# Performance work log

Hardware: AMD Instinct MI355X
Metric: run time of the kernel (lower is better)

The kernel has to match this reference:

```python
import jax, jax.numpy as jnp
import numpy as np

D_MODEL = 512
N_HEADS = 8
D_HEAD = D_MODEL // N_HEADS


def setup_inputs() -> dict:
    key = jax.random.key(0)
    ks = jax.random.split(key, 11)
    B, S = 2, 4096
    scale = 1.0 / np.sqrt(D_MODEL)
    inp = {
        "q": jax.random.normal(ks[0], (B, S, D_MODEL), dtype=jnp.float32),
        "k": jax.random.normal(ks[1], (B, S, D_MODEL), dtype=jnp.float32),
        "v": jax.random.normal(ks[2], (B, S, D_MODEL), dtype=jnp.float32),
        "Wq": jax.random.normal(ks[3], (D_MODEL, D_MODEL), dtype=jnp.float32) * scale,
        "bq": jnp.zeros((D_MODEL,), dtype=jnp.float32),
        "Wk": jax.random.normal(ks[4], (D_MODEL, D_MODEL), dtype=jnp.float32) * scale,
        "bk": jnp.zeros((D_MODEL,), dtype=jnp.float32),
        "Wv": jax.random.normal(ks[5], (D_MODEL, D_MODEL), dtype=jnp.float32) * scale,
        "bv": jnpp if False else jnp.zeros((D_MODEL,), dtype=jnp.float32),
        "Wo": jax.random.normal(ks[6], (D_MODEL, D_MODEL), dtype=jnp.float32) * scale,
        "bo": jnp.zeros((D_MODEL,), dtype=jnp.float32),
    }
    return inp


def reference(q, k, v, Wq, bq, Wk, bk, Wv, bv, Wo, bo):
    B, S, _ = q.shape
    # Linear projections (torch Linear: x @ W^T + b), split into heads -> [B,H,S,Dh]
    def proj(x, W, b):
        y = jnp.einsum("bsd,ed->bse", x, W) + b
        return y.reshape(B, -1, N_HEADS, D_HEAD).transpose(0, 2, 1, 3)

    Q = proj(q, Wq, bq)
    K = proj(k, Wk, bk)
    V = proj(v, Wv, bv)

    inv_sqrt_dh = 1.0 / np.sqrt(D_HEAD).astype(np.float32)
    scores = jnp.einsum("bhqd,bhkd->bhqk", Q, K) * inv_sqrt_dh  # [B,H,S,S]
    attn = jax.nn.softmax(scores, axis=-1)  # dropout is identity at eval
    out = jnp.einsum("bhqk,bhkd->bhqd", attn, V)  # [B,H,S,Dh]
    out = out.transpose(0, 2, 1, 3).reshape(B, S, D_MODEL)
    return jnp.einsum("bsd,ed->bse", out, Wo) + bo
```

## Files before the change

### kernel.cpp

```cpp
#include <hip/hip_runtime.h>
#include <hip/hip_bf16.h>
#include <hip/hip_fp16.h>
#include <stdint.h>

#define D_MODEL 512
#define NH 8
#define DH 64
#define BB 2
#define SS 4096
#define MTOT (BB*SS)
#define NJQ 2

typedef __attribute__((ext_vector_type(8))) short bf16x8;
typedef __attribute__((ext_vector_type(4))) float f32x4;
typedef __fp16 fp16x2 __attribute__((ext_vector_type(2)));

#define MFMA32(a,b,c) __builtin_amdgcn_mfma_f32_16x16x32_bf16(a,b,c,0,0,0)

#if __has_builtin(__builtin_amdgcn_exp2f)
  #define EXP2F(x) __builtin_amdgcn_exp2f(x)
#else
  #define EXP2F(x) __expf((x) * 0.6931471805599453f)
#endif

#define QSCALE 0.18033688011112042f
#define EXPOFF 11.541560327679939f

__device__ __forceinline__ unsigned f2b(float f) {
  return (__float_as_uint(f) + 0x8000u) >> 16;
}
__device__ __forceinline__ float h2f(unsigned short h) {
  return __half2float(__ushort_as_half(h));
}
__device__ __forceinline__ unsigned packh2(float lo, float hi) {
  fp16x2 h = __builtin_amdgcn_cvt_pkrtz(lo, hi);
  return __builtin_bit_cast(unsigned, h);
}
__device__ __forceinline__ unsigned packpair(float lo, float hi) {
  return __builtin_amdgcn_perm(__float_as_uint(hi) + 0x8000u,
                               __float_as_uint(lo) + 0x8000u, 0x07060302u);
}
__device__ __forceinline__ unsigned cvtpk_bf16(float lo, float hi) {
  unsigned r;
  asm("v_cvt_pk_bf16_f32 %0, %1, %2" : "=v"(r) : "v"(lo), "v"(hi));
  return r;
}
__device__ __forceinline__ void gload_lds16(const unsigned short* g, unsigned short* l) {
  __builtin_amdgcn_global_load_lds(
      (const __attribute__((address_space(1))) unsigned int*)g,
      (__attribute__((address_space(3))) unsigned int*)l, 16, 0, 0);
}

struct PrepArgs {
  const float* src[7];
  unsigned short* dst[7];
  int off[8];
};

__global__ __launch_bounds__(256) void prep_kernel(PrepArgs a) {
  const int bx = blockIdx.x;
  int tgt = 0;
#pragma unroll
  for (int s = 1; s < 7; s++) tgt += (bx >= a.off[s]);
  const int i = ((bx - a.off[tgt]) * 256 + threadIdx.x) * 8;
  const float4 f0 = *(const float4*)(a.src[tgt] + i);
  const float4 f1 = *(const float4*)(a.src[tgt] + i + 4);
  uint4 o;
  o.x = packpair(f0.x, f0.y);
  o.y = packpair(f0.z, f0.w);
  o.z = packpair(f1.x, f1.y);
  o.w = packpair(f1.z, f1.w);
  *(uint4*)(a.dst[tgt] + i) = o;
}

struct CombArgs {
  const unsigned short* Os[NJQ];
  const float* ls[NJQ];
  unsigned short* Ao;
};

__global__ __launch_bounds__(256) void combine_kernel(CombArgs c) {
  const size_t i = ((size_t)blockIdx.x * 256 + threadIdx.x) * 8;
  const int m = (int)(i >> 9);
  const int k = (int)(i & 511);
  const int hh = k >> 6;
  float lsum = 0.f;
#pragma unroll
  for (int s = 0; s < NJQ; s++) lsum += c.ls[s][(size_t)m * NH + hh];
  const float inv = __builtin_amdgcn_rcpf(lsum);
  float sum[8] = {0.f, 0.f, 0.f, 0.f, 0.f, 0.f, 0.f, 0.f};
#pragma unroll
  for (int s = 0; s < NJQ; s++) {
    uint4 hv = *(const uint4*)(c.Os[s] + i);
    const unsigned short* he = (const unsigned short*)&hv;
#pragma unroll
    for (int e = 0; e < 8; e++) sum[e] += h2f(he[e]);
  }
  uint4 pk;
  pk.x = packpair(sum[0] * inv, sum[1] * inv);
  pk.y = packpair(sum[2] * inv, sum[3] * inv);
  pk.z = packpair(sum[4] * inv, sum[5] * inv);
  pk.w = packpair(sum[6] * inv, sum[7] * inv);
  *(uint4*)(c.Ao + i) = pk;
}

struct GemmArgs {
  const unsigned short* A[3];
  const unsigned short* W[3];
  const float* bias[3];
  unsigned short* out[3];
  float* outf;
  int mode;
};

__global__ __launch_bounds__(256) void gemm_kernel(GemmArgs g) {
  const int z = blockIdx.z;
  const float* __restrict__ bias = g.bias[z];
  unsigned short* __restrict__ out = g.out[z];
  const bool vt = (g.mode == 0) && (z == 2);
  const float osc = (g.mode == 0 && z == 0) ? QSCALE : 1.0f;

  __shared__ __align__(128) unsigned short lA[128][32];
  __shared__ __align__(128) unsigned short lB[128][32];

  const int t = threadIdx.x;
  const int lane = t & 63;
  const int w = t >> 6;
  const int wr = w >> 1, wc = w & 1;
  const int lrow = lane & 15, quad = lane >> 4;

  const int ob = blockIdx.y * 4 + blockIdx.x;
  const int lid = (ob & 7) * 32 + (ob >> 3);
  const int m0 = (lid >> 2) * 128;
  const int n0 = (lid & 3) * 128;

  const int srow = lane >> 2;
  const int schunk = (lane & 3) * 8;

  const unsigned short* __restrict__ Ag = g.A[z];
  const unsigned short* __restrict__ Wg = g.W[z];

  f32x4 acc[4][4];
  for (int i = 0; i < 4; i++)
    for (int j = 0; j < 4; j++)
      for (int r = 0; r < 4; r++) acc[i][j][r] = 0.f;

  for (int kk = 0; kk < 512; kk += 32) {
#pragma unroll
    for (int i = 0; i < 2; i++) {
      const int r0 = w * 32 + i * 16;
      gload_lds16(Ag + (size_t)(m0 + r0 + srow) * 512 + kk + schunk, &lA[r0][0]);
      gload_lds16(Wg + (size_t)(n0 + r0 + srow) * 512 + kk + schunk, &lB[r0][0]);
    }
    __syncthreads();
    bf16x8 af[4], bfr[4];
#pragma unroll
    for (int mt = 0; mt < 4; mt++) af[mt] = *(const bf16x8*)&lA[wr * 64 + mt * 16 + lrow][quad * 8];
#pragma unroll
    for (int nt = 0; nt < 4; nt++) bfr[nt] = *(const bf16x8*)&lB[wc * 64 + nt * 16 + lrow][quad * 8];
#pragma unroll
    for (int mt = 0; mt < 4; mt++)
#pragma unroll
      for (int nt = 0; nt < 4; nt++)
        acc[mt][nt] = MFMA32(af[mt], bfr[nt], acc[mt][nt]);
    __syncthreads();
  }

  float bv[4];
#pragma unroll
  for (int nt = 0; nt < 4; nt++) bv[nt] = bias[n0 + wc * 64 + nt * 16 + lrow];

#pragma unroll
  for (int mt = 0; mt < 4; mt++) {
#pragma unroll
    for (int nt = 0; nt < 4; nt++) {
      const int n = n0 + wc * 64 + nt * 16 + lrow;
      const int mB = m0 + wr * 64 + mt * 16 + quad * 4;
      float val[4];
#pragma unroll
      for (int r = 0; r < 4; r++) val[r] = (acc[mt][nt][r] + bv[nt]) * osc;

      if (g.mode == 1) {
#pragma unroll
        for (int r = 0; r < 4; r++) g.outf[(size_t)(mB + r) * 512 + n] = val[r];
      } else if (vt) {
        const int bb = mB >> 12, s = mB & 4095;
        const int a = s >> 2;
        const int c0 = (s & ~31) + (a & 4) + ((a & 3) << 3);
        const int hh = n >> 6, dh = n & 63;
        ushort4 pk = make_ushort4((unsigned short)f2b(val[0]), (unsigned short)f2b(val[1]),
                                  (unsigned short)f2b(val[2]), (unsigned short)f2b(val[3]));
        *(ushort4*)(out + (((size_t)bb * NH + hh) * DH + dh) * SS + c0) = pk;
      } else {
        const int bb = mB >> 12;
        const int hh = n >> 6, dh = n & 63;
#pragma unroll
        for (int r = 0; r < 4; r++) {
          const int s = (mB + r) & 4095;
          out[((((size_t)bb * NH + hh) * SS + s) << 6) + dh] = (unsigned short)f2b(val[r]);
        }
      }
    }
  }
}

struct AttnArgs {
  const unsigned short* Qh;
  const unsigned short* Kh;
  const unsigned short* Vt;
  unsigned short* Op[NJQ];
  float* lp[NJQ];
};

__global__ __launch_bounds__(512, 4) void attn_kernel(AttnArgs a) {
  __shared__ __align__(16) unsigned short lK[64][72];
  __shared__ __align__(16) unsigned short lV[64][72];

  const int t = threadIdx.x;
  const int lane = t & 63;
  const int w = t >> 6;
  const int lrow = lane & 15, quad = lane >> 4;
  const int h = blockIdx.y, b = blockIdx.z;
  const int qtile = blockIdx.x & 15, jq = blockIdx.x >> 4;
  const size_t kb = ((size_t)b * NH + h) * SS * DH;
  const size_t vb = ((size_t)b * NH + h) * DH * SS;
  const int qrow0 = qtile * 256 + w * 32;
  unsigned short* __restrict__ Op = a.Op[jq];
  float* __restrict__ lp = a.lp[jq];
  const int jt0 = jq * 32, jt1 = jt0 + 32;

  bf16x8 qf[2][2];
#pragma unroll
  for (int ti = 0; ti < 2; ti++) {
    const unsigned short* qp = a.Qh + kb + (size_t)(qrow0 + ti * 16 + lrow) * DH + quad * 8;
    qf[ti][0] = *(const bf16x8*)qp;
    qf[ti][1] = *(const bf16x8*)(qp + 32);
  }

  f32x4 o[2][4];
  float lsum[2] = {0.f, 0.f};
#pragma unroll
  for (int ti = 0; ti < 2; ti++)
    for (int nt = 0; nt < 4; nt++)
      for (int r = 0; r < 4; r++) o[ti][nt][r] = 0.f;

  const unsigned short* __restrict__ Kg = a.Kh + kb;
  const unsigned short* __restrict__ Vg = a.Vt + vb;

  const int rk = t >> 3;
  const int ck = (t & 7) * 8;

  uint4 kreg = *(const uint4*)(Kg + (size_t)(jt0 * 64 + rk) * DH + ck);
  uint4 vreg = *(const uint4*)(Vg + (size_t)rk * SS + jt0 * 64 + ck);

  const f32x4 sinit = {-EXPOFF, -EXPOFF, -EXPOFF, -EXPOFF};

  for (int jt = jt0; jt < jt1; jt++) {
    __syncthreads();
    *(uint4*)&lK[rk][ck] = kreg;
    *(uint4*)&lV[rk][ck] = vreg;
    {
      const int nb = (jt + 1 < jt1 ? jt + 1 : jt) * 64;
      kreg = *(const uint4*)(Kg + (size_t)(nb + rk) * DH + ck);
      vreg = *(const uint4*)(Vg + (size_t)rk * SS + nb + ck);
    }
    __syncthreads();

#pragma unroll
    for (int half = 0; half < 2; half++) {
      uint2 pw[2][2];
#pragma unroll
      for (int u = 0; u < 2; u++) {
        const int ntj = half * 2 + u;
        bf16x8 k0 = *(const bf16x8*)&lK[ntj * 16 + lrow][quad * 8];
        bf16x8 k1 = *(const bf16x8*)&lK[ntj * 16 + lrow][32 + quad * 8];
#pragma unroll
        for (int ti = 0; ti < 2; ti++) {
          f32x4 s = MFMA32(k0, qf[ti][0], sinit);
          s = MFMA32(k1, qf[ti][1], s);
          const float e0 = EXP2F(s[0]);
          const float e1 = EXP2F(s[1]);
          const float e2 = EXP2F(s[2]);
          const float e3 = EXP2F(s[3]);
          lsum[ti] += (e0 + e1) + (e2 + e3);
          pw[u][ti].x = cvtpk_bf16(e0, e1);
          pw[u][ti].y = cvtpk_bf16(e2, e3);
        }
      }
      bf16x8 pcat[2];
#pragma unroll
      for (int ti = 0; ti < 2; ti++) {
        uint4 c;
        c.x = pw[0][ti].x; c.y = pw[0][ti].y;
        c.z = pw[1][ti].x; c.w = pw[1][ti].y;
        pcat[ti] = __builtin_bit_cast(bf16x8, c);
      }
#pragma unroll
      for (int nt = 0; nt < 4; nt++) {
        bf16x8 vv = *(const bf16x8*)&lV[nt * 16 + lrow][half * 32 + quad * 8];
#pragma unroll
        for (int ti = 0; ti < 2; ti++)
          o[ti][nt] = MFMA32(vv, pcat[ti], o[ti][nt]);
      }
    }
  }

#pragma unroll
  for (int ti = 0; ti < 2; ti++) {
    float l = lsum[ti];
    l += __shfl_xor(l, 16);
    l += __shfl_xor(l, 32);
    const int si = qrow0 + ti * 16 + lrow;
    unsigned short* dst = Op + ((size_t)(b * SS + si)) * D_MODEL + h * DH;
#pragma unroll
    for (int nt = 0; nt < 4; nt++) {
      uint2 pk;
      pk.x = packh2(o[ti][nt][0], o[ti][nt][1]);
      pk.y = packh2(o[ti][nt][2], o[ti][nt][3]);
      *(uint2*)(dst + nt * 16 + quad * 4) = pk;
    }
    if (quad == 0)
      lp[(size_t)(b * SS + si) * NH + h] = l;
  }
}

extern "C" void kernel_launch(void* const* d_in, const int* in_sizes, int n_in,
                              void* d_out, int out_size, void* d_ws, size_t ws_size,
                              hipStream_t stream) {
  const float* q  = (const float*)d_in[0];
  const float* k  = (const float*)d_in[1];
  const float* v  = (const float*)d_in[2];
  const float* Wq = (const float*)d_in[3];
  const float* bq = (const float*)d_in[4];
  const float* Wk = (const float*)d_in[5];
  const float* bk = (const float*)d_in[6];
  const float* Wv = (const float*)d_in[7];
  const float* bv = (const float*)d_in[8];
  const float* Wo = (const float*)d_in[9];
  const float* bo = (const float*)d_in[10];

  const size_t NX = (size_t)MTOT * D_MODEL;
  const size_t NW = (size_t)D_MODEL * D_MODEL;

  char* p = (char*)d_ws;
  unsigned short* qb  = (unsigned short*)p; p += NX * 2;
  unsigned short* kbf = (unsigned short*)p; p += NX * 2;
  unsigned short* vbf = (unsigned short*)p; p += NX * 2;
  unsigned short* Wqb = (unsigned short*)p; p += NW * 2;
  unsigned short* Wkb = (unsigned short*)p; p += NW * 2;
  unsigned short* Wvb = (unsigned short*)p; p += NW * 2;
  unsigned short* Wob = (unsigned short*)p; p += NW * 2;
  unsigned short* Qh  = (unsigned short*)p; p += NX * 2;
  unsigned short* Kh  = (unsigned short*)p; p += NX * 2;
  unsigned short* Vtg = (unsigned short*)p; p += NX * 2;
  unsigned short* Ao  = (unsigned short*)p; p += NX * 2;
  unsigned short* Os[NJQ];
  float* ls[NJQ];
  for (int i = 0; i < NJQ; i++) { Os[i] = (unsigned short*)p; p += NX * 2; }
  for (int i = 0; i < NJQ; i++) { ls[i] = (float*)p; p += (size_t)MTOT * NH * 4; }

  PrepArgs pr;
  pr.src[0] = q;  pr.dst[0] = qb;
  pr.src[1] = k;  pr.dst[1] = kbf;
  pr.src[2] = v;  pr.dst[2] = vbf;
  pr.src[3] = Wq; pr.dst[3] = Wqb;
  pr.src[4] = Wk; pr.dst[4] = Wkb;
  pr.src[5] = Wv; pr.dst[5] = Wvb;
  pr.src[6] = Wo; pr.dst[6] = Wob;
  {
    const int nb[7] = {(int)(NX / 2048), (int)(NX / 2048), (int)(NX / 2048),
                       (int)(NW / 2048), (int)(NW / 2048), (int)(NW / 2048),
                       (int)(NW / 2048)};
    int acc = 0;
    for (int i = 0; i < 7; i++) { pr.off[i] = acc; acc += nb[i]; }
    pr.off[7] = acc;
    prep_kernel<<<dim3(acc, 1, 1), 256, 0, stream>>>(pr);
  }

  GemmArgs pa;
  pa.A[0] = qb; pa.A[1] = kbf; pa.A[2] = vbf;
  pa.W[0] = Wqb; pa.W[1] = Wkb; pa.W[2] = Wvb;
  pa.bias[0] = bq; pa.bias[1] = bk; pa.bias[2] = bv;
  pa.out[0] = Qh; pa.out[1] = Kh; pa.out[2] = Vtg;
  pa.outf = nullptr;
  pa.mode = 0;
  gemm_kernel<<<dim3(4, 64, 3), 256, 0, stream>>>(pa);

  AttnArgs aa;
  aa.Qh = Qh; aa.Kh = Kh; aa.Vt = Vtg;
  for (int i = 0; i < NJQ; i++) { aa.Op[i] = Os[i]; aa.lp[i] = ls[i]; }
  attn_kernel<<<dim3(16 * NJQ, NH, BB), 512, 0, stream>>>(aa);

  CombArgs ca;
  for (int i = 0; i < NJQ; i++) { ca.Os[i] = Os[i]; ca.ls[i] = ls[i]; }
  ca.Ao = Ao;
  combine_kernel<<<dim3((int)(NX / 8 / 256), 1, 1), 256, 0, stream>>>(ca);

  GemmArgs oa;
  oa.A[0] = Ao; oa.A[1] = Ao; oa.A[2] = Ao;
  oa.W[0] = Wob; oa.W[1] = Wob; oa.W[2] = Wob;
  oa.bias[0] = bo; oa.bias[1] = bo; oa.bias[2] = bo;
  oa.out[0] = nullptr; oa.out[1] = nullptr; oa.out[2] = nullptr;
  oa.outf = (float*)d_out;
  oa.mode = 1;
  gemm_kernel<<<dim3(4, 64, 1), 256, 0, stream>>>(oa);
}
```

Before: 223.8 us.

## Drop key-range split and fuse softmax normalization into attention epilogue

The attention kernel now walks all 64 key tiles in a single block instead of splitting the key range into two halves. It normalizes the output by the row sum in its own epilogue and writes bf16 straight to the output-projection input. This removes the separate combine kernel, its launch, and the partial-output and row-sum buffers along with their global traffic. In exchange the attention grid halves to 256 blocks, about one per CU, so fewer waves are resident per CU to hide latency.

```diff
diff --git a/kernel.cpp b/kernel.cpp
--- a/kernel.cpp
+++ b/kernel.cpp
@@ -9,7 +9,6 @@
 #define BB 2
 #define SS 4096
 #define MTOT (BB*SS)
-#define NJQ 2
 
 typedef __attribute__((ext_vector_type(8))) short bf16x8;
 typedef __attribute__((ext_vector_type(4))) float f32x4;
@@ -71,37 +70,6 @@
   o.z = packpair(f1.x, f1.y);
   o.w = packpair(f1.z, f1.w);
   *(uint4*)(a.dst[tgt] + i) = o;
-}
-
-struct CombArgs {
-  const unsigned short* Os[NJQ];
-  const float* ls[NJQ];
-  unsigned short* Ao;
-};
-
-__global__ __launch_bounds__(256) void combine_kernel(CombArgs c) {
-  const size_t i = ((size_t)blockIdx.x * 256 + threadIdx.x) * 8;
-  const int m = (int)(i >> 9);
-  const int k = (int)(i & 511);
-  const int hh = k >> 6;
-  float lsum = 0.f;
-#pragma unroll
-  for (int s = 0; s < NJQ; s++) lsum += c.ls[s][(size_t)m * NH + hh];
-  const float inv = __builtin_amdgcn_rcpf(lsum);
-  float sum[8] = {0.f, 0.f, 0.f, 0.f, 0.f, 0.f, 0.f, 0.f};
-#pragma unroll
-  for (int s = 0; s < NJQ; s++) {
-    uint4 hv = *(const uint4*)(c.Os[s] + i);
-    const unsigned short* he = (const unsigned short*)&hv;
-#pragma unroll
-    for (int e = 0; e < 8; e++) sum[e] += h2f(he[e]);
-  }
-  uint4 pk;
-  pk.x = packpair(sum[0] * inv, sum[1] * inv);
-  pk.y = packpair(sum[2] * inv, sum[3] * inv);
-  pk.z = packpair(sum[4] * inv, sum[5] * inv);
-  pk.w = packpair(sum[6] * inv, sum[7] * inv);
-  *(uint4*)(c.Ao + i) = pk;
 }
 
 struct GemmArgs {
@@ -208,8 +176,7 @@
   const unsigned short* Qh;
   const unsigned short* Kh;
   const unsigned short* Vt;
-  unsigned short* Op[NJQ];
-  float* lp[NJQ];
+  unsigned short* Ao;
 };
 
 __global__ __launch_bounds__(512, 4) void attn_kernel(AttnArgs a) {
@@ -221,13 +188,10 @@
   const int w = t >> 6;
   const int lrow = lane & 15, quad = lane >> 4;
   const int h = blockIdx.y, b = blockIdx.z;
-  const int qtile = blockIdx.x & 15, jq = blockIdx.x >> 4;
+  const int qtile = blockIdx.x;
   const size_t kb = ((size_t)b * NH + h) * SS * DH;
   const size_t vb = ((size_t)b * NH + h) * DH * SS;
   const int qrow0 = qtile * 256 + w * 32;
-  unsigned short* __restrict__ Op = a.Op[jq];
-  float* __restrict__ lp = a.lp[jq];
-  const int jt0 = jq * 32, jt1 = jt0 + 32;
 
   bf16x8 qf[2][2];
 #pragma unroll
@@ -250,17 +214,17 @@
   const int rk = t >> 3;
   const int ck = (t & 7) * 8;
 
-  uint4 kreg = *(const uint4*)(Kg + (size_t)(jt0 * 64 + rk) * DH + ck);
-  uint4 vreg = *(const uint4*)(Vg + (size_t)rk * SS + jt0 * 64 + ck);
+  uint4 kreg = *(const uint4*)(Kg + (size_t)rk * DH + ck);
+  uint4 vreg = *(const uint4*)(Vg + (size_t)rk * SS + ck);
 
   const f32x4 sinit = {-EXPOFF, -EXPOFF, -EXPOFF, -EXPOFF};
 
-  for (int jt = jt0; jt < jt1; jt++) {
+  for (int jt = 0; jt < 64; jt++) {
     __syncthreads();
     *(uint4*)&lK[rk][ck] = kreg;
     *(uint4*)&lV[rk][ck] = vreg;
     {
-      const int nb = (jt + 1 < jt1 ? jt + 1 : jt) * 64;
+      const int nb = (jt + 1 < 64 ? jt + 1 : jt) * 64;
       kreg = *(const uint4*)(Kg + (size_t)(nb + rk) * DH + ck);
       vreg = *(const uint4*)(Vg + (size_t)rk * SS + nb + ck);
     }
@@ -310,17 +274,16 @@
     float l = lsum[ti];
     l += __shfl_xor(l, 16);
     l += __shfl_xor(l, 32);
+    const float inv = __builtin_amdgcn_rcpf(l);
     const int si = qrow0 + ti * 16 + lrow;
-    unsigned short* dst = Op + ((size_t)(b * SS + si)) * D_MODEL + h * DH;
+    unsigned short* dst = a.Ao + ((size_t)(b * SS + si)) * D_MODEL + h * DH;
 #pragma unroll
     for (int nt = 0; nt < 4; nt++) {
       uint2 pk;
-      pk.x = packh2(o[ti][nt][0], o[ti][nt][1]);
-      pk.y = packh2(o[ti][nt][2], o[ti][nt][3]);
+      pk.x = cvtpk_bf16(o[ti][nt][0] * inv, o[ti][nt][1] * inv);
+      pk.y = cvtpk_bf16(o[ti][nt][2] * inv, o[ti][nt][3] * inv);
       *(uint2*)(dst + nt * 16 + quad * 4) = pk;
     }
-    if (quad == 0)
-      lp[(size_t)(b * SS + si) * NH + h] = l;
   }
 }
 
@@ -354,10 +317,6 @@
   unsigned short* Kh  = (unsigned short*)p; p += NX * 2;
   unsigned short* Vtg = (unsigned short*)p; p += NX * 2;
   unsigned short* Ao  = (unsigned short*)p; p += NX * 2;
-  unsigned short* Os[NJQ];
-  float* ls[NJQ];
-  for (int i = 0; i < NJQ; i++) { Os[i] = (unsigned short*)p; p += NX * 2; }
-  for (int i = 0; i < NJQ; i++) { ls[i] = (float*)p; p += (size_t)MTOT * NH * 4; }
 
   PrepArgs pr;
   pr.src[0] = q;  pr.dst[0] = qb;
@@ -387,14 +346,8 @@
   gemm_kernel<<<dim3(4, 64, 3), 256, 0, stream>>>(pa);
 
   AttnArgs aa;
-  aa.Qh = Qh; aa.Kh = Kh; aa.Vt = Vtg;
-  for (int i = 0; i < NJQ; i++) { aa.Op[i] = Os[i]; aa.lp[i] = ls[i]; }
-  attn_kernel<<<dim3(16 * NJQ, NH, BB), 512, 0, stream>>>(aa);
-
-  CombArgs ca;
-  for (int i = 0; i < NJQ; i++) { ca.Os[i] = Os[i]; ca.ls[i] = ls[i]; }
-  ca.Ao = Ao;
-  combine_kernel<<<dim3((int)(NX / 8 / 256), 1, 1), 256, 0, stream>>>(ca);
+  aa.Qh = Qh; aa.Kh = Kh; aa.Vt = Vtg; aa.Ao = Ao;
+  attn_kernel<<<dim3(16, NH, BB), 512, 0, stream>>>(aa);
 
   GemmArgs oa;
   oa.A[0] = Ao; oa.A[1] = Ao; oa.A[2] = Ao;
```

New measurement: 214.3 us. 4.3% less time.
